# Kernel optimization log

Hardware: AMD Instinct MI355X
Metric: run time of the kernel (lower is better)

Reference implementation:

```python
import jax, jax.numpy as jnp
import numpy as np

D_MODEL, D_K, D_V, N_HEADS = 1024, 64, 64, 16
B, S = 2, 2048
LN_EPS = 1e-5


def setup_inputs() -> dict:
    key = jax.random.key(0)
    ks = jax.random.split(key, 12)
    s = 1.0 / np.sqrt(D_MODEL)
    inp = {
        "Q": jax.random.normal(ks[0], (B, S, D_MODEL), jnp.float32),
        "K": jax.random.normal(ks[1], (B, S, D_MODEL), jnp.float32),
        "V": jax.random.normal(ks[2], (B, S, D_MODEL), jnp.float32),
        "attn_mask": jax.random.bernoulli(ks[3], 0.1, (B, S, S)),
        "Wq": jax.random.uniform(ks[4], (D_MODEL, D_K * N_HEADS), jnp.float32, -s, s),
        "bq": jnp.zeros((D_K * N_HEADS,), jnp.float32),
        "Wk": jax.random.uniform(ks[5], (D_MODEL, D_K * N_HEADS), jnp.float32, -s, s),
        "bk": jnp.zeros((D_K * N_HEADS,), jnp.float32),
        "Wv": jax.random.uniform(ks[6], (D_MODEL, D_V * N_HEADS), jnp.float32, -s, s),
        "bv": jnp.zeros((D_V * N_HEADS,), jnp.float32),
        "Wo": jax.random.uniform(ks[7], (N_HEADS * D_V, D_MODEL), jnp.float32, -s, s),
        "bo": jnp.zeros((D_MODEL,), jnp.float32),
        "gamma": jnp.ones((D_MODEL,), jnp.float32),
        "beta": jnp.zeros((D_MODEL,), jnp.float32),
    }
    return inp


def reference(Q, K, V, attn_mask, Wq, bq, Wk, bk, Wv, bv, Wo, bo, gamma, beta):
    b, s, _ = Q.shape
    # projections -> [B, S, H, d]
    q = (Q @ Wq + bq).reshape(b, s, N_HEADS, D_K)
    k = (K @ Wk + bk).reshape(b, -1, N_HEADS, D_K)
    v = (V @ Wv + bv).reshape(b, -1, N_HEADS, D_V)
    # scores [B, H, Sq, Sk]
    scores = jnp.einsum("bqhd,bkhd->bhqk", q, k) / np.sqrt(D_K).astype(np.float32)
    scores = jnp.where(attn_mask[:, None, :, :], jnp.float32(-1e9), scores)
    attn = jax.nn.softmax(scores, axis=-1)
    context = jnp.einsum("bhqk,bkhd->bqhd", attn, v).reshape(b, s, N_HEADS * D_V)
    out = context @ Wo + bo + Q  # residual
    mu = jnp.mean(out, axis=-1, keepdims=True)
    var = jnp.var(out, axis=-1, keepdims=True)
    return (out - mu) * jax.lax.rsqrt(var + LN_EPS) * gamma + beta
```

## Files before the change

kernel.cpp:

```cpp
#include <hip/hip_runtime.h>
#include <hip/hip_bf16.h>
#include <math.h>


#define D_MODEL 1024
#define NHEADS  16
#define DHEAD   64
#define BATCH   2
#define SEQ     2048
#define MROWS   (BATCH * SEQ)
#define SCLF    0.18033688f

typedef __attribute__((ext_vector_type(8)))  short bf16x8;
typedef __attribute__((ext_vector_type(4)))  float f32x4;
typedef __attribute__((ext_vector_type(16))) float f32x16;

__device__ inline unsigned short f2bf(float f) {
    unsigned int u = __builtin_bit_cast(unsigned int, f);
    unsigned int r = (u + 0x7FFFu + ((u >> 16) & 1u)) >> 16;
    return (unsigned short)r;
}

__device__ inline unsigned cvtpk_bf16(float lo, float hi2) {
    unsigned r;
    asm("v_cvt_pk_bf16_f32 %0, %1, %2" : "=v"(r) : "v"(lo), "v"(hi2));
    return r;
}

__device__ inline void gload16(const unsigned short* g, unsigned short* lbase, int lane) {
#if __has_builtin(__builtin_amdgcn_global_load_lds)
    __builtin_amdgcn_global_load_lds(
        (const __attribute__((address_space(1))) unsigned int*)g,
        (__attribute__((address_space(3))) unsigned int*)lbase, 16, 0, 0);
#else
    *(bf16x8*)(lbase + lane * 8) = *(const bf16x8*)g;
#endif
}

__global__ __launch_bounds__(256) void detect_mask_par(
    const unsigned int* __restrict__ m, int nwords, int* __restrict__ flags)
{
    const int i = blockIdx.x * 256 + threadIdx.x;
    int a = 0, b = 0;
    if (i < nwords) {
        const unsigned int w = m[i];
        a = (w != 0u && w != 1u);
        b = (w != 0u && w != 0x3F800000u);
    }
    const int wa = (int)__any(a);
    const int wb = (int)__any(b);
    if ((threadIdx.x & 63) == 0) {
        if (wa) atomicOr(&flags[0], 1);
        if (wb) atomicOr(&flags[1], 1);
    }
}

__global__ __launch_bounds__(256) void pack_mask_ballot(
    const void* __restrict__ mask, const int* __restrict__ flags,
    unsigned long long* __restrict__ mbits, int nwords)
{
    const int lane   = threadIdx.x & 63;
    const int wv     = blockIdx.x * 4 + (threadIdx.x >> 6);
    const int nwaves = gridDim.x * 4;
    const int mf = (flags[0] == 0) ? 0 : (flags[1] == 0) ? 1 : 2;
    for (int w = wv; w < nwords; w += nwaves) {
        bool bit;
        if (mf == 0)      bit = ((const unsigned int*)mask)[(size_t)w * 64 + lane] != 0u;
        else if (mf == 1) bit = ((const float*)mask)[(size_t)w * 64 + lane] != 0.f;
        else              bit = ((const unsigned char*)mask)[(size_t)w * 64 + lane] != 0;
        const unsigned long long b = __ballot(bit);
        if (lane == 0) mbits[w] = b;
    }
}

__global__ __launch_bounds__(256) void cvt_all(
    const float* __restrict__ Q, const float* __restrict__ K,
    const float* __restrict__ V,
    const float* __restrict__ w0, const float* __restrict__ w1,
    const float* __restrict__ w2, const float* __restrict__ w3,
    unsigned short* __restrict__ Qb, unsigned short* __restrict__ Kb,
    unsigned short* __restrict__ Vb,
    unsigned short* __restrict__ t0, unsigned short* __restrict__ t1,
    unsigned short* __restrict__ t2, unsigned short* __restrict__ t3)
{
    __shared__ float tile[64][65];
    const int z = blockIdx.z;
    if (z < 3) {
        const float* s = (z == 0) ? Q : (z == 1) ? K : V;
        unsigned short* d = (z == 0) ? Qb : (z == 1) ? Kb : Vb;
        const int i = blockIdx.x * 256 + threadIdx.x;
        float4 a = ((const float4*)s)[i * 2];
        float4 b = ((const float4*)s)[i * 2 + 1];
        unsigned u0 = cvtpk_bf16(a.x, a.y);
        unsigned u1 = cvtpk_bf16(a.z, a.w);
        unsigned u2 = cvtpk_bf16(b.x, b.y);
        unsigned u3 = cvtpk_bf16(b.z, b.w);
        ((int4*)d)[i] = make_int4((int)u0, (int)u1, (int)u2, (int)u3);
    } else {
        if (blockIdx.x >= 256) return;
        const int wz = z - 3;
        const float* W = (wz == 0) ? w0 : (wz == 1) ? w1 : (wz == 2) ? w2 : w3;
        unsigned short* T = (wz == 0) ? t0 : (wz == 1) ? t1 : (wz == 2) ? t2 : t3;
        const int n0 = (blockIdx.x & 15) * 64;
        const int k0 = (blockIdx.x >> 4) * 64;
        const int t  = threadIdx.x;
        const int r  = t >> 4;
        const int c4 = (t & 15) * 4;
        #pragma unroll
        for (int u = 0; u < 4; ++u) {
            float4 v = *(const float4*)(W + (size_t)(k0 + r + u * 16) * D_MODEL + n0 + c4);
            tile[r + u * 16][c4 + 0] = v.x;
            tile[r + u * 16][c4 + 1] = v.y;
            tile[r + u * 16][c4 + 2] = v.z;
            tile[r + u * 16][c4 + 3] = v.w;
        }
        __syncthreads();
        #pragma unroll
        for (int u = 0; u < 4; ++u) {
            const int nr = r + u * 16;
            ushort4 o;
            o.x = f2bf(tile[c4 + 0][nr]);
            o.y = f2bf(tile[c4 + 1][nr]);
            o.z = f2bf(tile[c4 + 2][nr]);
            o.w = f2bf(tile[c4 + 3][nr]);
            *(ushort4*)(T + (size_t)(n0 + nr) * D_MODEL + k0 + c4) = o;
        }
    }
}

#define BKQ 32
__global__ __launch_bounds__(256, 1) void gemm_qkv(
    const unsigned short* __restrict__ A0, const unsigned short* __restrict__ A1,
    const unsigned short* __restrict__ A2,
    const unsigned short* __restrict__ B0, const unsigned short* __restrict__ B1,
    const unsigned short* __restrict__ B2,
    const float* __restrict__ bias0, const float* __restrict__ bias1,
    const float* __restrict__ bias2,
    unsigned short* __restrict__ C0, unsigned short* __restrict__ C1,
    unsigned short* __restrict__ C2)
{
    const int z = blockIdx.z;
    const unsigned short* A  = (z == 0) ? A0 : (z == 1) ? A1 : A2;
    const unsigned short* Bt = (z == 0) ? B0 : (z == 1) ? B1 : B2;
    const float* bias        = (z == 0) ? bias0 : (z == 1) ? bias1 : bias2;
    unsigned short* C        = (z == 0) ? C0 : (z == 1) ? C1 : C2;
    const int K = D_MODEL, N = D_MODEL;

    __shared__ unsigned short As[2][128 * BKQ];
    __shared__ unsigned short Bs[2][128 * BKQ];
    const int tid  = threadIdx.x;
    const int w    = tid >> 6;
    const int lane = tid & 63;
    const int lo   = lane & 15;
    const int hi   = lane >> 4;
    const int wm   = (w >> 1) * 64;
    const int wn   = (w & 1) * 64;
    const int m0   = blockIdx.x * 128;
    const int n0   = blockIdx.y * 128;

    const unsigned short* Ab = A  + (size_t)m0 * K;
    const unsigned short* Bb = Bt + (size_t)n0 * K;

    f32x4 acc[4][4];
    #pragma unroll
    for (int i = 0; i < 4; ++i)
        #pragma unroll
        for (int j = 0; j < 4; ++j) acc[i][j] = (f32x4){0.f, 0.f, 0.f, 0.f};

    const int NT = K / BKQ;
    auto stage = [&](int buf, int t) {
        const int k0 = t * BKQ;
        #pragma unroll
        for (int i = 0; i < 2; ++i) {
            const int c = i * 256 + tid;
            gload16(Ab + (size_t)(c >> 2) * K + k0 + (c & 3) * 8,
                    &As[buf][(i * 256 + w * 64) * 8], lane);
        }
        #pragma unroll
        for (int i = 0; i < 2; ++i) {
            const int c = i * 256 + tid;
            gload16(Bb + (size_t)(c >> 2) * K + k0 + (c & 3) * 8,
                    &Bs[buf][(i * 256 + w * 64) * 8], lane);
        }
    };

    stage(0, 0);
    __syncthreads();
    int cur = 0;
    for (int t = 0; t < NT; ++t) {
        if (t + 1 < NT) stage(cur ^ 1, t + 1);
        bf16x8 af[4], bfr[4];
        #pragma unroll
        for (int f = 0; f < 4; ++f) {
            af[f]  = *(const bf16x8*)&As[cur][(wm + f * 16 + lo) * BKQ + hi * 8];
            bfr[f] = *(const bf16x8*)&Bs[cur][(wn + f * 16 + lo) * BKQ + hi * 8];
        }
        #pragma unroll
        for (int fm = 0; fm < 4; ++fm)
            #pragma unroll
            for (int fn = 0; fn < 4; ++fn)
                acc[fm][fn] = __builtin_amdgcn_mfma_f32_16x16x32_bf16(
                    af[fm], bfr[fn], acc[fm][fn], 0, 0, 0);
        __syncthreads();
        cur ^= 1;
    }

    #pragma unroll
    for (int fm = 0; fm < 4; ++fm) {
        const int row = m0 + wm + fm * 16 + hi * 4;
        #pragma unroll
        for (int fn = 0; fn < 4; ++fn) {
            const int col = n0 + wn + fn * 16 + lo;
            const float bv = bias[col];
            #pragma unroll
            for (int r = 0; r < 4; ++r) {
                float o = acc[fm][fn][r] + bv;
                if (z == 0) o *= SCLF;
                if (z < 2)
                    C[(size_t)(row + r) * N + col] = f2bf(o);
                else
                    C[(size_t)((row + r) >> 11) * 2097152
                      + (size_t)col * 2048 + ((row + r) & 2047)] = f2bf(o);
            }
        }
    }
}

#define BKK 64
__global__ __launch_bounds__(256) void gemm_out64(
    const unsigned short* __restrict__ A, const unsigned short* __restrict__ Bt,
    const float* __restrict__ bias, const float* __restrict__ resid,
    float* __restrict__ C)
{
    const int K = D_MODEL, N = D_MODEL;
    __shared__ unsigned short As[2][128 * BKK];
    __shared__ unsigned short Bs[2][64 * BKK];
    const int tid  = threadIdx.x;
    const int w    = tid >> 6;
    const int lane = tid & 63;
    const int lo   = lane & 15;
    const int hi   = lane >> 4;
    const int wm   = (w >> 1) * 64;
    const int wn   = (w & 1) * 32;
    const int m0   = blockIdx.x * 128;
    const int n0   = blockIdx.y * 64;

    const unsigned short* Ab = A  + (size_t)m0 * K;
    const unsigned short* Bb = Bt + (size_t)n0 * K;

    f32x4 acc[4][2];
    #pragma unroll
    for (int i = 0; i < 4; ++i)
        #pragma unroll
        for (int j = 0; j < 2; ++j) acc[i][j] = (f32x4){0.f, 0.f, 0.f, 0.f};

    const int NT = K / BKK;
    auto stage = [&](int buf, int t) {
        const int k0 = t * BKK;
        #pragma unroll
        for (int i = 0; i < 4; ++i) {
            const int c = i * 256 + tid;
            gload16(Ab + (size_t)(c >> 3) * K + k0 + (c & 7) * 8,
                    &As[buf][(i * 256 + w * 64) * 8], lane);
        }
        #pragma unroll
        for (int i = 0; i < 2; ++i) {
            const int c = i * 256 + tid;
            gload16(Bb + (size_t)(c >> 3) * K + k0 + (c & 7) * 8,
                    &Bs[buf][(i * 256 + w * 64) * 8], lane);
        }
    };

    stage(0, 0);
    __syncthreads();
    int cur = 0;
    for (int t = 0; t < NT; ++t) {
        if (t + 1 < NT) stage(cur ^ 1, t + 1);
        bf16x8 af[4][2], bfr[2][2];
        #pragma unroll
        for (int f = 0; f < 4; ++f)
            #pragma unroll
            for (int s = 0; s < 2; ++s)
                af[f][s] = *(const bf16x8*)&As[cur][(wm + f * 16 + lo) * BKK + s * 32 + hi * 8];
        #pragma unroll
        for (int f = 0; f < 2; ++f)
            #pragma unroll
            for (int s = 0; s < 2; ++s)
                bfr[f][s] = *(const bf16x8*)&Bs[cur][(wn + f * 16 + lo) * BKK + s * 32 + hi * 8];
        #pragma unroll
        for (int s = 0; s < 2; ++s)
            #pragma unroll
            for (int fm = 0; fm < 4; ++fm)
                #pragma unroll
                for (int fn = 0; fn < 2; ++fn)
                    acc[fm][fn] = __builtin_amdgcn_mfma_f32_16x16x32_bf16(
                        af[fm][s], bfr[fn][s], acc[fm][fn], 0, 0, 0);
        __syncthreads();
        cur ^= 1;
    }

    #pragma unroll
    for (int fm = 0; fm < 4; ++fm) {
        const int row = m0 + wm + fm * 16 + hi * 4;
        #pragma unroll
        for (int fn = 0; fn < 2; ++fn) {
            const int col = n0 + wn + fn * 16 + lo;
            const float bv = bias[col];
            #pragma unroll
            for (int r = 0; r < 4; ++r)
                C[(size_t)(row + r) * N + col] =
                    acc[fm][fn][r] + bv + resid[(size_t)(row + r) * N + col];
        }
    }
}

__global__ __launch_bounds__(512, 2) void attn_mfma32(
    const unsigned short* __restrict__ qb, const unsigned short* __restrict__ kbm,
    const unsigned short* __restrict__ vt,
    const unsigned long long* __restrict__ mbits, unsigned short* __restrict__ ctx)
{
    __shared__ __align__(16) unsigned char smem[34304];
    const int tid  = threadIdx.x;
    const int w8   = tid >> 6;
    const int g    = w8 >> 2;
    const int wq   = w8 & 3;
    const int lane = tid & 63;
    const int l31  = lane & 31;
    const int hi   = lane >> 5;
    const int h    = blockIdx.x;
    const int q0   = blockIdx.y * 128;
    const int b    = blockIdx.z;

    unsigned short* KsG = (unsigned short*)smem + (size_t)g * 4096;
    unsigned short* VsG = (unsigned short*)(smem + 16384) + (size_t)g * 4096;

    const size_t qkbase = (size_t)b * SEQ * D_MODEL + (size_t)h * DHEAD;
    const size_t vtbase = ((size_t)b * D_MODEL + h * DHEAD) * SEQ;

    const int qtok = q0 + wq * 32 + l31;
    bf16x8 qA[4];
    #pragma unroll
    for (int s = 0; s < 4; ++s)
        qA[s] = *(const bf16x8*)(qb + qkbase + (size_t)qtok * D_MODEL + s * 16 + hi * 8);

    const int4 ones_i = make_int4(0x3F803F80, 0x3F803F80, 0x3F803F80, 0x3F803F80);
    const bf16x8 ones = __builtin_bit_cast(bf16x8, ones_i);

    f32x16 o0 = {}, o1 = {}, accl = {};

    const unsigned long long* mrow = mbits + ((size_t)b * SEQ + qtok) * (SEQ / 64);

    const int krow = wq * 8 + (lane >> 3);
    const int kc   = lane & 7;
    const int kswz = kc ^ (krow & 7);
    const int vrow = wq * 16 + (lane >> 2);
    const int vsrc = ((lane & 3) - (vrow >> 1)) & 3;

    const unsigned short* kl = kbm + qkbase + (size_t)(g * 1024 + krow) * D_MODEL + kswz * 8;
    const unsigned short* vl = vt + vtbase + (size_t)vrow * SEQ + g * 1024 + vsrc * 8;
    const int kldb = (wq * 8) * 64;
    const int vldb = (wq * 16) * 32;

    auto stage = [&](int buf) {
        gload16(kl, &KsG[buf * 2048 + kldb], lane);
        gload16(vl, &VsG[buf * 2048 + vldb], lane);
        kl += (size_t)32 * D_MODEL;
        vl += 32;
    };

    stage(0);
    unsigned long long mw64 = mrow[g * 16];
    __syncthreads();
    int cur = 0;

    for (int t = 0; t < 32; ++t) {
        if (t + 1 < 32) stage(cur ^ 1);
        const unsigned int mw = (unsigned int)(mw64 >> (32 * (t & 1) + 4 * hi));
        if ((t & 1) && t + 1 < 32) mw64 = mrow[g * 16 + ((t + 1) >> 1)];

        f32x16 st = {};
        __builtin_amdgcn_s_setprio(1);
        #pragma unroll
        for (int s = 0; s < 4; ++s) {
            bf16x8 kf = *(const bf16x8*)&KsG[cur * 2048 + l31 * 64 + ((2 * s + hi) ^ (l31 & 7)) * 8];
            st = __builtin_amdgcn_mfma_f32_32x32x16_bf16(kf, qA[s], st, 0, 0, 0);
        }
        __builtin_amdgcn_s_setprio(0);

        #pragma unroll
        for (int r = 0; r < 16; ++r) {
            const int klo = (r & 3) + 8 * (r >> 2);
            const float x = ((mw >> klo) & 1u) ? -1e9f : st[r];
            st[r] = exp2f(x);
        }

        bf16x8 pa[2];
        #pragma unroll
        for (int s = 0; s < 2; ++s) {
            const int base = s * 8;
            unsigned av  = cvtpk_bf16(st[base + 0], st[base + 1]);
            unsigned bv2 = cvtpk_bf16(st[base + 4], st[base + 5]);
            unsigned cv  = cvtpk_bf16(st[base + 2], st[base + 3]);
            unsigned dv  = cvtpk_bf16(st[base + 6], st[base + 7]);
            asm("v_permlane32_swap_b32 %0, %1" : "+v"(av), "+v"(bv2));
            asm("v_permlane32_swap_b32 %0, %1" : "+v"(cv), "+v"(dv));
            int4 pk = make_int4((int)av, (int)cv, (int)bv2, (int)dv);
            pa[s] = __builtin_bit_cast(bf16x8, pk);
        }

        __builtin_amdgcn_s_setprio(1);
        #pragma unroll
        for (int s = 0; s < 2; ++s) {
            const int slot = ((2 * s + hi) + (l31 >> 1)) & 3;
            bf16x8 vf0 = *(const bf16x8*)&VsG[cur * 2048 + l31 * 32 + slot * 8];
            o0 = __builtin_amdgcn_mfma_f32_32x32x16_bf16(pa[s], vf0, o0, 0, 0, 0);
            bf16x8 vf1 = *(const bf16x8*)&VsG[cur * 2048 + (32 + l31) * 32 + slot * 8];
            o1 = __builtin_amdgcn_mfma_f32_32x32x16_bf16(pa[s], vf1, o1, 0, 0, 0);
            accl = __builtin_amdgcn_mfma_f32_32x32x16_bf16(pa[s], ones, accl, 0, 0, 0);
        }
        __builtin_amdgcn_s_setprio(0);
        __syncthreads();
        cur ^= 1;
    }

    __syncthreads();
    float* comb  = (float*)smem;
    float* lvals = (float*)(smem + 33792);
    if (g == 1) {
        float* p = comb + (size_t)(wq * 64 + lane) * 33;
        #pragma unroll
        for (int r = 0; r < 16; ++r) { p[r] = o0[r]; p[16 + r] = o1[r]; }
        if (l31 == 0) {
            #pragma unroll
            for (int r = 0; r < 16; ++r)
                lvals[wq * 32 + (r & 3) + 8 * (r >> 2) + 4 * hi] = accl[r];
        }
    }
    __syncthreads();
    if (g == 0) {
        const float* p = comb + (size_t)(wq * 64 + lane) * 33;
        #pragma unroll
        for (int r = 0; r < 16; ++r) {
            const int qloc = (r & 3) + 8 * (r >> 2) + 4 * hi;
            const float inv = 1.f / (accl[r] + lvals[wq * 32 + qloc]);
            unsigned short* dst = ctx + qkbase + (size_t)(q0 + wq * 32 + qloc) * D_MODEL;
            dst[l31]      = f2bf((o0[r] + p[r]) * inv);
            dst[32 + l31] = f2bf((o1[r] + p[16 + r]) * inv);
        }
    }
}

__global__ __launch_bounds__(256) void layernorm1024(
    const float* __restrict__ x, const float* __restrict__ gamma,
    const float* __restrict__ beta, float* __restrict__ out)
{
    const int row = blockIdx.x;
    const int tid = threadIdx.x;
    const float* xr = x + (size_t)row * D_MODEL;
    float4 v = *(const float4*)(xr + (tid << 2));
    float s = v.x + v.y + v.z + v.w;
    float q = v.x * v.x + v.y * v.y + v.z * v.z + v.w * v.w;
    #pragma unroll
    for (int off = 1; off < 64; off <<= 1) {
        s += __shfl_xor(s, off, 64);
        q += __shfl_xor(q, off, 64);
    }
    __shared__ float sw[4], qw_[4];
    const int wid = tid >> 6;
    if ((tid & 63) == 0) { sw[wid] = s; qw_[wid] = q; }
    __syncthreads();
    s = sw[0] + sw[1] + sw[2] + sw[3];
    q = qw_[0] + qw_[1] + qw_[2] + qw_[3];
    const float mu  = s * (1.f / D_MODEL);
    const float var = q * (1.f / D_MODEL) - mu * mu;
    const float a = var + 1e-5f;
    float inv = rsqrtf(a);
    inv = inv * (1.5f - 0.5f * a * inv * inv);
    float4 gg = *(const float4*)(gamma + (tid << 2));
    float4 bt = *(const float4*)(beta + (tid << 2));
    float4 o;
    o.x = (v.x - mu) * inv * gg.x + bt.x;
    o.y = (v.y - mu) * inv * gg.y + bt.y;
    o.z = (v.z - mu) * inv * gg.z + bt.z;
    o.w = (v.w - mu) * inv * gg.w + bt.w;
    *(float4*)(out + (size_t)row * D_MODEL + (tid << 2)) = o;
}

extern "C" void kernel_launch(void* const* d_in, const int* in_sizes, int n_in,
                              void* d_out, int out_size, void* d_ws, size_t ws_size,
                              hipStream_t stream)
{
    const float* Q    = (const float*)d_in[0];
    const float* K    = (const float*)d_in[1];
    const float* V    = (const float*)d_in[2];
    const void*  mask = d_in[3];
    const float* Wq   = (const float*)d_in[4];
    const float* bq   = (const float*)d_in[5];
    const float* Wk   = (const float*)d_in[6];
    const float* bk   = (const float*)d_in[7];
    const float* Wv   = (const float*)d_in[8];
    const float* bv   = (const float*)d_in[9];
    const float* Wo   = (const float*)d_in[10];
    const float* bo   = (const float*)d_in[11];
    const float* gam  = (const float*)d_in[12];
    const float* bet  = (const float*)d_in[13];
    float* out = (float*)d_out;

    const size_t NE = (size_t)MROWS * D_MODEL;
    const size_t WE = (size_t)D_MODEL * D_MODEL;
    const size_t NMW = (size_t)BATCH * SEQ * (SEQ / 64);
    unsigned short* Qbf = (unsigned short*)d_ws;
    unsigned short* Kbf = Qbf + NE;
    unsigned short* Vbf = Kbf + NE;
    unsigned short* qb  = Vbf + NE;
    unsigned short* kb  = qb + NE;
    unsigned short* vt  = kb + NE;
    unsigned short* Wt0 = vt + NE;
    unsigned short* Wt1 = Wt0 + WE;
    unsigned short* Wt2 = Wt1 + WE;
    unsigned short* Wt3 = Wt2 + WE;
    unsigned long long* mbits = (unsigned long long*)(Wt3 + WE);
    int* mflags = (int*)(mbits + NMW);
    unsigned short* ctxb = Qbf;
    float* outp = (float*)Kbf;
    if (ws_size < 6 * NE * 2 + 4 * WE * 2 + NMW * 8 + 64) return;

    hipMemsetAsync(mflags, 0, 2 * sizeof(int), stream);
    detect_mask_par<<<256, 256, 0, stream>>>((const unsigned int*)mask, 65536, mflags);
    pack_mask_ballot<<<2048, 256, 0, stream>>>(mask, mflags, mbits, (int)NMW);

    cvt_all<<<dim3(2048, 1, 7), 256, 0, stream>>>(Q, K, V, Wq, Wk, Wv, Wo,
                                                  Qbf, Kbf, Vbf, Wt0, Wt1, Wt2, Wt3);

    gemm_qkv<<<dim3(32, 8, 3), 256, 0, stream>>>(Qbf, Kbf, Vbf, Wt0, Wt1, Wt2,
                                                 bq, bk, bv, qb, kb, vt);

    dim3 ag(NHEADS, SEQ / 128, BATCH);
    attn_mfma32<<<ag, 512, 0, stream>>>(qb, kb, vt, mbits, ctxb);

    gemm_out64<<<dim3(32, 16), 256, 0, stream>>>(ctxb, Wt3, bo, Q, outp);

    layernorm1024<<<MROWS, 256, 0, stream>>>(outp, gam, bet, out);
}
```

Measured before the change: 180.1 us.

## Deepen attention K/V pipeline to four LDS buffers with explicit vmcnt waits

Expands the attention kernel's shared-memory K/V staging from double to quad buffering, prefetching two tiles ahead. The per-iteration __syncthreads is replaced by explicit s_waitcnt vmcnt counts plus a raw s_barrier, so more global-to-LDS loads stay in flight while the MFMA work runs. The mask bits for the whole row are preloaded into registers up front instead of being loaded mid-loop, and the loop is fully unrolled. LDS per block grows to 64KB, which may reduce occupancy with launch_bounds(512,2), and the larger unrolled body raises register pressure.

```diff
diff --git a/kernel.cpp b/kernel.cpp
--- a/kernel.cpp
+++ b/kernel.cpp
@@ -14,6 +14,8 @@
 typedef __attribute__((ext_vector_type(8)))  short bf16x8;
 typedef __attribute__((ext_vector_type(4)))  float f32x4;
 typedef __attribute__((ext_vector_type(16))) float f32x16;
+
+#define WAITV(n) asm volatile("s_waitcnt vmcnt(" #n ")" ::: "memory")
 
 __device__ inline unsigned short f2bf(float f) {
     unsigned int u = __builtin_bit_cast(unsigned int, f);
@@ -319,7 +321,7 @@
     const unsigned short* __restrict__ vt,
     const unsigned long long* __restrict__ mbits, unsigned short* __restrict__ ctx)
 {
-    __shared__ __align__(16) unsigned char smem[34304];
+    __shared__ __align__(16) unsigned char smem[65536];
     const int tid  = threadIdx.x;
     const int w8   = tid >> 6;
     const int g    = w8 >> 2;
@@ -331,8 +333,8 @@
     const int q0   = blockIdx.y * 128;
     const int b    = blockIdx.z;
 
-    unsigned short* KsG = (unsigned short*)smem + (size_t)g * 4096;
-    unsigned short* VsG = (unsigned short*)(smem + 16384) + (size_t)g * 4096;
+    unsigned short* KsG = (unsigned short*)smem + (size_t)g * 8192;
+    unsigned short* VsG = (unsigned short*)(smem + 32768) + (size_t)g * 8192;
 
     const size_t qkbase = (size_t)b * SEQ * D_MODEL + (size_t)h * DHEAD;
     const size_t vtbase = ((size_t)b * D_MODEL + h * DHEAD) * SEQ;
@@ -343,12 +345,19 @@
     for (int s = 0; s < 4; ++s)
         qA[s] = *(const bf16x8*)(qb + qkbase + (size_t)qtok * D_MODEL + s * 16 + hi * 8);
 
+    const unsigned long long* mrowg =
+        mbits + ((size_t)b * SEQ + qtok) * (SEQ / 64) + g * 16;
+    unsigned long long mall[16];
+    #pragma unroll
+    for (int i = 0; i < 8; ++i) {
+        ulonglong2 v = ((const ulonglong2*)mrowg)[i];
+        mall[2 * i] = v.x; mall[2 * i + 1] = v.y;
+    }
+
     const int4 ones_i = make_int4(0x3F803F80, 0x3F803F80, 0x3F803F80, 0x3F803F80);
     const bf16x8 ones = __builtin_bit_cast(bf16x8, ones_i);
 
     f32x16 o0 = {}, o1 = {}, accl = {};
-
-    const unsigned long long* mrow = mbits + ((size_t)b * SEQ + qtok) * (SEQ / 64);
 
     const int krow = wq * 8 + (lane >> 3);
     const int kc   = lane & 7;
@@ -368,21 +377,33 @@
         vl += 32;
     };
 
-    stage(0);
-    unsigned long long mw64 = mrow[g * 16];
-    __syncthreads();
-    int cur = 0;
-
+    WAITV(0);
+    __builtin_amdgcn_sched_barrier(0);
+    stage(0); stage(1);
+    WAITV(2);
+    __builtin_amdgcn_sched_barrier(0);
+    __builtin_amdgcn_s_barrier();
+    __builtin_amdgcn_sched_barrier(0);
+
+    #pragma unroll
     for (int t = 0; t < 32; ++t) {
-        if (t + 1 < 32) stage(cur ^ 1);
-        const unsigned int mw = (unsigned int)(mw64 >> (32 * (t & 1) + 4 * hi));
-        if ((t & 1) && t + 1 < 32) mw64 = mrow[g * 16 + ((t + 1) >> 1)];
+        if (t + 2 < 32) stage((t + 2) & 3);
+        if (t < 30)       { WAITV(4); }
+        else if (t == 30) { WAITV(2); }
+        else              { WAITV(0); }
+        __builtin_amdgcn_sched_barrier(0);
+        __builtin_amdgcn_s_barrier();
+        __builtin_amdgcn_sched_barrier(0);
+
+        const int buf = t & 3;
+        const unsigned int mw =
+            (unsigned int)(mall[t >> 1] >> (32 * (t & 1) + 4 * hi));
 
         f32x16 st = {};
         __builtin_amdgcn_s_setprio(1);
         #pragma unroll
         for (int s = 0; s < 4; ++s) {
-            bf16x8 kf = *(const bf16x8*)&KsG[cur * 2048 + l31 * 64 + ((2 * s + hi) ^ (l31 & 7)) * 8];
+            bf16x8 kf = *(const bf16x8*)&KsG[buf * 2048 + l31 * 64 + ((2 * s + hi) ^ (l31 & 7)) * 8];
             st = __builtin_amdgcn_mfma_f32_32x32x16_bf16(kf, qA[s], st, 0, 0, 0);
         }
         __builtin_amdgcn_s_setprio(0);
@@ -412,15 +433,13 @@
         #pragma unroll
         for (int s = 0; s < 2; ++s) {
             const int slot = ((2 * s + hi) + (l31 >> 1)) & 3;
-            bf16x8 vf0 = *(const bf16x8*)&VsG[cur * 2048 + l31 * 32 + slot * 8];
+            bf16x8 vf0 = *(const bf16x8*)&VsG[buf * 2048 + l31 * 32 + slot * 8];
             o0 = __builtin_amdgcn_mfma_f32_32x32x16_bf16(pa[s], vf0, o0, 0, 0, 0);
-            bf16x8 vf1 = *(const bf16x8*)&VsG[cur * 2048 + (32 + l31) * 32 + slot * 8];
+            bf16x8 vf1 = *(const bf16x8*)&VsG[buf * 2048 + (32 + l31) * 32 + slot * 8];
             o1 = __builtin_amdgcn_mfma_f32_32x32x16_bf16(pa[s], vf1, o1, 0, 0, 0);
             accl = __builtin_amdgcn_mfma_f32_32x32x16_bf16(pa[s], ones, accl, 0, 0, 0);
         }
         __builtin_amdgcn_s_setprio(0);
-        __syncthreads();
-        cur ^= 1;
     }
 
     __syncthreads();
```

Result: slower. 189.6 us (+5.2%).
